# Optimization experiments

Hardware: AMD Instinct MI355X
Metric: run time of the kernel (lower is better)

## Reference

```python
import jax, jax.numpy as jnp
import numpy as np

D = 1024      # n_embd
H = 16        # n_head
HD = D // H   # head_size = 64


def _layernorm(x, g, b, eps=1e-5):
    mu = jnp.mean(x, axis=-1, keepdims=True)
    var = jnp.mean((x - mu) ** 2, axis=-1, keepdims=True)
    return (x - mu) * jax.lax.rsqrt(var + eps) * g + b


def setup_inputs() -> dict:
    key = jax.random.key(0)
    ks = jax.random.split(key, 12)
    s = lambda fan_in: 1.0 / np.sqrt(fan_in)
    inp = {
        "x": jax.random.normal(ks[0], (4, 2048, D), dtype=jnp.float32),
        # attention projections (bias=False in Head), per-head weights fused into [D, D]
        "wq": jax.random.uniform(ks[1], (D, D), jnp.float32, -s(D), s(D)),
        "wk": jax.random.uniform(ks[2], (D, D), jnp.float32, -s(D), s(D)),
        "wv": jax.random.uniform(ks[3], (D, D), jnp.float32, -s(D), s(D)),
        "wo": jax.random.uniform(ks[4], (D, D), jnp.float32, -s(D), s(D)),
        "bo": jax.random.uniform(ks[5], (D,), jnp.float32, -s(D), s(D)),
        # feed-forward: D -> 4D -> D
        "w1": jax.random.uniform(ks[6], (D, 4 * D), jnp.float32, -s(D), s(D)),
        "b1": jax.random.uniform(ks[7], (4 * D,), jnp.float32, -s(D), s(D)),
        "w2": jax.random.uniform(ks[8], (4 * D, D), jnp.float32, -s(4 * D), s(4 * D)),
        "b2": jax.random.uniform(ks[9], (D,), jnp.float32, -s(4 * D), s(4 * D)),
        # layernorms
        "g_ln1": jnp.ones((D,), jnp.float32),
        "b_ln1": jnp.zeros((D,), jnp.float32),
        "g_ln2": jnp.ones((D,), jnp.float32),
        "b_ln2": jnp.zeros((D,), jnp.float32),
    }
    return inp


def reference(x, wq, wk, wv, wo, bo, w1, b1, w2, b2, g_ln1, b_ln1, g_ln2, b_ln2):
    B, T, _ = x.shape
    # --- self-attention on ln1(x) ---
    h = _layernorm(x, g_ln1, b_ln1)
    q = (h @ wq).reshape(B, T, H, HD)
    k = (h @ wk).reshape(B, T, H, HD)
    v = (h @ wv).reshape(B, T, H, HD)
    scores = jnp.einsum("bqhd,bkhd->bhqk", q, k) * (HD ** -0.5)
    causal = jnp.tril(jnp.ones((T, T), dtype=bool))
    scores = jnp.where(causal, scores, -jnp.inf)
    wei = jax.nn.softmax(scores, axis=-1)                    # [B,H,T,T]
    attn = jnp.einsum("bhqk,bkhd->bqhd", wei, v).reshape(B, T, D)
    x = x + attn @ wo + bo
    # --- feed-forward on ln2(x) ---
    h2 = _layernorm(x, g_ln2, b_ln2)
    x = x + jax.nn.relu(h2 @ w1 + b1) @ w2 + b2
    return x
```

## Files before the change

### kernel.cpp

```cpp
#include <hip/hip_runtime.h>
#include <cstdint>

typedef __bf16 bf16x8 __attribute__((ext_vector_type(8)));
typedef float f32x4 __attribute__((ext_vector_type(4)));
typedef unsigned int u32x4 __attribute__((ext_vector_type(4)));
typedef unsigned int u32x2 __attribute__((ext_vector_type(2)));
typedef unsigned short u16x4 __attribute__((ext_vector_type(4)));

#define D_MODEL 1024
#define SEQ     2048
#define NBATCH  4
#define NHEAD   16
#define HDIM    64
#define NTOK    (NBATCH * SEQ)
#define QSCALE  0.18033688011112042f

__device__ __forceinline__ unsigned short f2bf(float f) {
  unsigned int u = __builtin_bit_cast(unsigned int, f);
  u += 0x7FFFu + ((u >> 16) & 1u);
  return (unsigned short)(u >> 16);
}

__device__ __forceinline__ float bf2f(unsigned short s) {
  return __builtin_bit_cast(float, (unsigned int)s << 16);
}

__device__ __forceinline__ bf16x8 load8bf(const unsigned short* p) {
  return __builtin_bit_cast(bf16x8, *(const u32x4*)p);
}

__device__ __forceinline__ f32x4 mfma16(bf16x8 a, bf16x8 b, f32x4 c) {
  return __builtin_amdgcn_mfma_f32_16x16x32_bf16(a, b, c, 0, 0, 0);
}

__device__ __forceinline__ void gload16(const unsigned short* g, unsigned short* l) {
  __builtin_amdgcn_global_load_lds((__attribute__((address_space(1))) void*)g,
                                   (__attribute__((address_space(3))) void*)l, 16, 0, 0);
}

__global__ __launch_bounds__(256) void tcast_all(const float* __restrict__ wq,
                                                 const float* __restrict__ wk,
                                                 const float* __restrict__ wv,
                                                 const float* __restrict__ wo,
                                                 const float* __restrict__ w1,
                                                 const float* __restrict__ w2,
                                                 unsigned short* __restrict__ wqkv_t,
                                                 unsigned short* __restrict__ wo_t,
                                                 unsigned short* __restrict__ w1_t,
                                                 unsigned short* __restrict__ w2_t) {
  const int id = blockIdx.x;
  const float* in; unsigned short* out; int K, N, k0, n0;
  if (id < 4096) {
    const int seg = id >> 10, r = id & 1023;
    in  = seg == 0 ? wq : seg == 1 ? wk : seg == 2 ? wv : wo;
    out = seg == 3 ? wo_t : wqkv_t + (size_t)seg * 1024 * 1024;
    K = 1024; N = 1024; n0 = (r & 31) * 32; k0 = (r >> 5) * 32;
  } else if (id < 8192) {
    const int r = id - 4096;
    in = w1; out = w1_t; K = 1024; N = 4096;
    n0 = (r & 127) * 32; k0 = (r >> 7) * 32;
  } else {
    const int r = id - 8192;
    in = w2; out = w2_t; K = 4096; N = 1024;
    n0 = (r & 31) * 32; k0 = (r >> 5) * 32;
  }
  __shared__ float tile[32][33];
  const int tx = threadIdx.x & 31, ty = threadIdx.x >> 5;
  #pragma unroll
  for (int j = 0; j < 4; ++j)
    tile[ty + 8 * j][tx] = in[(size_t)(k0 + ty + 8 * j) * N + n0 + tx];
  __syncthreads();
  #pragma unroll
  for (int j = 0; j < 4; ++j)
    out[(size_t)(n0 + ty + 8 * j) * K + k0 + tx] = f2bf(tile[tx][ty + 8 * j]);
}

template <int FPIN>
__global__ __launch_bounds__(256) void ln_kernel(const void* __restrict__ xin,
                                                 const float* __restrict__ g,
                                                 const float* __restrict__ bb,
                                                 unsigned short* __restrict__ out) {
  const int row = blockIdx.x, tid = threadIdx.x;
  float4 xv;
  if (FPIN) {
    xv = ((const float4*)((const float*)xin + (size_t)row * D_MODEL))[tid];
  } else {
    const u16x4 bv4 = ((const u16x4*)((const unsigned short*)xin + (size_t)row * D_MODEL))[tid];
    xv.x = bf2f(bv4.x); xv.y = bf2f(bv4.y); xv.z = bf2f(bv4.z); xv.w = bf2f(bv4.w);
  }
  float s  = xv.x + xv.y + xv.z + xv.w;
  float ss = xv.x * xv.x + xv.y * xv.y + xv.z * xv.z + xv.w * xv.w;
  #pragma unroll
  for (int off = 1; off < 64; off <<= 1) { s += __shfl_xor(s, off); ss += __shfl_xor(ss, off); }
  __shared__ float red[8];
  const int wave = tid >> 6, lane = tid & 63;
  if (lane == 0) { red[wave] = s; red[4 + wave] = ss; }
  __syncthreads();
  s  = red[0] + red[1] + red[2] + red[3];
  ss = red[4] + red[5] + red[6] + red[7];
  const float mu   = s * (1.0f / D_MODEL);
  const float var  = ss * (1.0f / D_MODEL) - mu * mu;
  const float rstd = rsqrtf(var + 1e-5f);
  const float4 gv = ((const float4*)g)[tid];
  const float4 bv = ((const float4*)bb)[tid];
  u16x4 o;
  o.x = f2bf((xv.x - mu) * rstd * gv.x + bv.x);
  o.y = f2bf((xv.y - mu) * rstd * gv.y + bv.y);
  o.z = f2bf((xv.z - mu) * rstd * gv.z + bv.z);
  o.w = f2bf((xv.w - mu) * rstd * gv.w + bv.w);
  *(u16x4*)(out + (size_t)row * D_MODEL + tid * 4) = o;
}

template <bool BIAS, bool RELU, int RES, bool OBF>
__global__ __launch_bounds__(256) void gemm_bt(const unsigned short* __restrict__ A,
                                               const unsigned short* __restrict__ Bt,
                                               const float* __restrict__ bias,
                                               const void* __restrict__ res,
                                               void* __restrict__ out,
                                               int M, int N, int K) {
  __shared__ __align__(16) unsigned short As[128 * 64];
  __shared__ __align__(16) unsigned short Bs[128 * 64];
  const int tid  = threadIdx.x;
  const int lin = blockIdx.y * gridDim.x + blockIdx.x;
  const int xcd = lin & 7, idx = lin >> 3;
  const int by = xcd * 8 + (idx & 7);
  const int bx = idx >> 3;
  const int row0 = by * 128, col0 = bx * 128;
  const int wave = tid >> 6, lane = tid & 63;
  const int wm = wave >> 1, wn = wave & 1;
  const int l15 = lane & 15, quad = lane >> 4;
  f32x4 acc[4][4] = {};

  const int tr = tid >> 3;
  const int tc = (tid & 7) ^ (tr & 7);
  const unsigned short* gA = A  + (size_t)(row0 + tr) * K + tc * 8;
  const unsigned short* gB = Bt + (size_t)(col0 + tr) * K + tc * 8;

  const int rowA = (wm * 64 + l15) * 64;
  const int rowB = (wn * 64 + l15) * 64;
  const int swz0 = (quad ^ (l15 & 7)) * 8;
  const int swz1 = ((4 + quad) ^ (l15 & 7)) * 8;

  for (int k0 = 0; k0 < K; k0 += 64) {
    #pragma unroll
    for (int i = 0; i < 4; ++i) {
      gload16(gA + (size_t)(i * 32) * K + k0, As + (i * 256 + tid) * 8);
      gload16(gB + (size_t)(i * 32) * K + k0, Bs + (i * 256 + tid) * 8);
    }
    __syncthreads();
    #pragma unroll
    for (int kf = 0; kf < 2; ++kf) {
      const int swz = kf ? swz1 : swz0;
      bf16x8 af[4], bfr[4];
      #pragma unroll
      for (int t = 0; t < 4; ++t) {
        af[t]  = load8bf(As + rowA + t * 1024 + swz);
        bfr[t] = load8bf(Bs + rowB + t * 1024 + swz);
      }
      #pragma unroll
      for (int i = 0; i < 4; ++i)
        #pragma unroll
        for (int j = 0; j < 4; ++j)
          acc[i][j] = mfma16(af[i], bfr[j], acc[i][j]);
    }
    __syncthreads();
  }

  const size_t rbase = (size_t)row0 + wm * 64 + quad * 4;
  const int cbase = col0 + wn * 64 + l15;
  #pragma unroll
  for (int i = 0; i < 4; ++i) {
    #pragma unroll
    for (int j = 0; j < 4; ++j) {
      const int col = cbase + j * 16;
      const float bval = BIAS ? bias[col] : 0.0f;
      #pragma unroll
      for (int r = 0; r < 4; ++r) {
        const size_t row = rbase + i * 16 + r;
        float v = acc[i][j][r];
        if (BIAS) v += bval;
        if (RELU) v = fmaxf(v, 0.0f);
        if (RES == 1) v += ((const float*)res)[row * N + col];
        if (RES == 2) v += bf2f(((const unsigned short*)res)[row * N + col]);
        if (OBF)  ((unsigned short*)out)[row * N + col] = f2bf(v);
        else      ((float*)out)[row * N + col] = v;
      }
    }
  }
}

__device__ __forceinline__ void stage_half_512(const unsigned short* __restrict__ src,
                                               unsigned short* dst, int ld, int k0,
                                               int h, int tid) {
  #pragma unroll
  for (int l = 0; l < 2; ++l) {
    const int cid = l * 512 + tid;
    const int r = cid >> 3, p = cid & 7, c = p ^ (r & 7);
    gload16(src + (size_t)(h * 128 + r) * ld + k0 + c * 8, dst + h * 8192 + cid * 8);
  }
}

template <bool BIAS, bool RELU, int RES, bool OBF, bool QKV, bool SPLITK>
__global__ __launch_bounds__(512, 2) void gemm256(const unsigned short* __restrict__ A,
                                                  const unsigned short* __restrict__ Bt,
                                                  const float* __restrict__ bias,
                                                  const void* __restrict__ res,
                                                  void* __restrict__ out,
                                                  unsigned short* __restrict__ qb,
                                                  unsigned short* __restrict__ kp,
                                                  unsigned short* __restrict__ vt,
                                                  int M, int N, int K, int lda, int ldb) {
  __shared__ __align__(16) unsigned short lds[2][32768];
  const int tid = threadIdx.x;
  const int lin = blockIdx.y * gridDim.x + blockIdx.x;
  const int xcd = lin & 7, idx = lin >> 3;
  const int by = xcd * 4 + (idx & 3);
  const int bxr = idx >> 2;
  const int ks  = SPLITK ? (bxr >> 2) : 0;
  const int bx  = SPLITK ? (bxr & 3) : bxr;
  const int row0 = by * 256, col0 = bx * 256;
  const int koff = SPLITK ? ks * K : 0;
  const int wave = tid >> 6, lane = tid & 63;
  const int wm = wave >> 2, wn = wave & 3;
  const int l15 = lane & 15, quad = lane >> 4;
  const int swz0 = (quad ^ (l15 & 7)) * 8;
  const int swz1 = ((4 + quad) ^ (l15 & 7)) * 8;

  const unsigned short* gA = A  + (size_t)row0 * lda + koff;
  const unsigned short* gB = Bt + (size_t)col0 * ldb + koff;

  unsigned short* As0 = &lds[0][0];
  unsigned short* Bs0 = &lds[0][16384];
  unsigned short* As1 = &lds[1][0];
  unsigned short* Bs1 = &lds[1][16384];

  f32x4 acc[8][4] = {};
  const int KT = K >> 6;

  stage_half_512(gA, As0, lda, 0, 0, tid);
  stage_half_512(gA, As0, lda, 0, 1, tid);
  stage_half_512(gB, Bs0, ldb, 0, 0, tid);
  stage_half_512(gB, Bs0, ldb, 0, 1, tid);
  if (KT > 1) {
    stage_half_512(gB, Bs1, ldb, 64, 0, tid);
    stage_half_512(gB, Bs1, ldb, 64, 1, tid);
    asm volatile("s_waitcnt vmcnt(4)" ::: "memory");
  } else {
    asm volatile("s_waitcnt vmcnt(0)" ::: "memory");
  }
  asm volatile("s_barrier" ::: "memory");

  for (int t = 0; t < KT; ++t) {
    unsigned short* As  = (t & 1) ? As1 : As0;
    unsigned short* Bs  = (t & 1) ? Bs1 : Bs0;
    unsigned short* Asn = (t & 1) ? As0 : As1;
    const int k1 = (t + 1) << 6, k2 = (t + 2) << 6;
    bf16x8 a0[2][4], b01[2][2], b23[2][2];

    #pragma unroll
    for (int i = 0; i < 4; ++i) {
      const unsigned short* ap = As + (wm * 128 + i * 16 + l15) * 64;
      a0[0][i] = load8bf(ap + swz0);
      a0[1][i] = load8bf(ap + swz1);
    }
    #pragma unroll
    for (int j = 0; j < 2; ++j) {
      const unsigned short* bp = Bs + (wn * 64 + j * 16 + l15) * 64;
      b01[0][j] = load8bf(bp + swz0);
      b01[1][j] = load8bf(bp + swz1);
      const unsigned short* bp2 = Bs + (wn * 64 + 32 + j * 16 + l15) * 64;
      b23[0][j] = load8bf(bp2 + swz0);
      b23[1][j] = load8bf(bp2 + swz1);
    }
    if (t + 1 < KT) {
      stage_half_512(gA, Asn, lda, k1, 0, tid);
      stage_half_512(gA, Asn, lda, k1, 1, tid);
    }
    __builtin_amdgcn_s_setprio(1);
    #pragma unroll
    for (int kf = 0; kf < 2; ++kf)
      #pragma unroll
      for (int i = 0; i < 4; ++i)
        #pragma unroll
        for (int j = 0; j < 2; ++j)
          acc[i][j] = mfma16(a0[kf][i], b01[kf][j], acc[i][j]);
    #pragma unroll
    for (int kf = 0; kf < 2; ++kf)
      #pragma unroll
      for (int i = 0; i < 4; ++i)
        #pragma unroll
        for (int j = 0; j < 2; ++j)
          acc[i][2 + j] = mfma16(a0[kf][i], b23[kf][j], acc[i][2 + j]);
    __builtin_amdgcn_s_setprio(0);
    __builtin_amdgcn_sched_barrier(0);
    asm volatile("s_barrier" ::: "memory");

    #pragma unroll
    for (int i = 0; i < 4; ++i) {
      const unsigned short* ap = As + (wm * 128 + 64 + i * 16 + l15) * 64;
      a0[0][i] = load8bf(ap + swz0);
      a0[1][i] = load8bf(ap + swz1);
    }
    if (t + 2 < KT) {
      stage_half_512(gB, Bs, ldb, k2, 0, tid);
      stage_half_512(gB, Bs, ldb, k2, 1, tid);
    }
    __builtin_amdgcn_s_setprio(1);
    #pragma unroll
    for (int kf = 0; kf < 2; ++kf)
      #pragma unroll
      for (int i = 0; i < 4; ++i)
        #pragma unroll
        for (int j = 0; j < 2; ++j)
          acc[4 + i][2 + j] = mfma16(a0[kf][i], b23[kf][j], acc[4 + i][2 + j]);
    #pragma unroll
    for (int kf = 0; kf < 2; ++kf)
      #pragma unroll
      for (int i = 0; i < 4; ++i)
        #pragma unroll
        for (int j = 0; j < 2; ++j)
          acc[4 + i][j] = mfma16(a0[kf][i], b01[kf][j], acc[4 + i][j]);
    __builtin_amdgcn_s_setprio(0);
    __builtin_amdgcn_sched_barrier(0);
    if (t + 2 < KT) asm volatile("s_waitcnt vmcnt(4)" ::: "memory");
    else            asm volatile("s_waitcnt vmcnt(0)" ::: "memory");
    asm volatile("s_barrier" ::: "memory");
  }

  const size_t rbase = (size_t)row0 + wm * 128 + quad * 4;
  const int cbase = col0 + wn * 64 + l15;
  if (QKV) {
    const int sec = col0 >> 10;
    #pragma unroll
    for (int i = 0; i < 8; ++i) {
      #pragma unroll
      for (int j = 0; j < 4; ++j) {
        const int col = cbase + j * 16;
        if (sec == 0) {
          #pragma unroll
          for (int r = 0; r < 4; ++r) {
            const size_t row = rbase + i * 16 + r;
            qb[row * 1024 + col] = f2bf(acc[i][j][r] * QSCALE);
          }
        } else if (sec == 1) {
          const int c2 = col - 1024, hh = c2 >> 6, d = c2 & 63;
          #pragma unroll
          for (int r = 0; r < 4; ++r) {
            const size_t row = rbase + i * 16 + r;
            const int bb = (int)(row >> 11), tt = (int)(row & 2047);
            kp[(((size_t)(bb * 16 + hh)) * SEQ + tt) * 64 + d] = f2bf(acc[i][j][r]);
          }
        } else {
          const int c2 = col - 2048, hh = c2 >> 6, d = c2 & 63;
          const size_t t0 = rbase + i * 16;
          const int bb = (int)(t0 >> 11);
          u16x4 pk;
          #pragma unroll
          for (int r = 0; r < 4; ++r) pk[r] = f2bf(acc[i][j][r]);
          *(u16x4*)(vt + ((size_t)(bb * 16 + hh) * 64 + d) * SEQ + (t0 & 2047)) = pk;
        }
      }
    }
  } else if (SPLITK) {
    float* po = (float*)out + (size_t)ks * M * N;
    #pragma unroll
    for (int i = 0; i < 8; ++i) {
      #pragma unroll
      for (int j = 0; j < 4; ++j) {
        const int col = cbase + j * 16;
        #pragma unroll
        for (int r = 0; r < 4; ++r) {
          const size_t row = rbase + i * 16 + r;
          po[row * N + col] = acc[i][j][r];
        }
      }
    }
  } else {
    #pragma unroll
    for (int i = 0; i < 8; ++i) {
      #pragma unroll
      for (int j = 0; j < 4; ++j) {
        const int col = cbase + j * 16;
        const float bval = BIAS ? bias[col] : 0.0f;
        #pragma unroll
        for (int r = 0; r < 4; ++r) {
          const size_t row = rbase + i * 16 + r;
          float v = acc[i][j][r];
          if (BIAS) v += bval;
          if (RELU) v = fmaxf(v, 0.0f);
          if (RES == 1) v += ((const float*)res)[row * N + col];
          if (RES == 2) v += bf2f(((const unsigned short*)res)[row * N + col]);
          if (OBF)  ((unsigned short*)out)[row * N + col] = f2bf(v);
          else      ((float*)out)[row * N + col] = v;
        }
      }
    }
  }
  (void)M;
}

__global__ __launch_bounds__(256) void ffn2_reduce(const float* __restrict__ p0,
                                                   const float* __restrict__ p1,
                                                   const float* __restrict__ b2,
                                                   const unsigned short* __restrict__ x1b,
                                                   float* __restrict__ out) {
  const size_t i4 = (size_t)blockIdx.x * 256 + threadIdx.x;
  const float4 a = ((const float4*)p0)[i4];
  const float4 b = ((const float4*)p1)[i4];
  const float4 bi = ((const float4*)b2)[i4 & 255];
  const u16x4 rv = ((const u16x4*)x1b)[i4];
  float4 o;
  o.x = a.x + b.x + bi.x + bf2f(rv.x);
  o.y = a.y + b.y + bi.y + bf2f(rv.y);
  o.z = a.z + b.z + bi.z + bf2f(rv.z);
  o.w = a.w + b.w + bi.w + bf2f(rv.w);
  ((float4*)out)[i4] = o;
}

__global__ __launch_bounds__(256) void attn5(const unsigned short* __restrict__ qb,
                                             const unsigned short* __restrict__ kp,
                                             const unsigned short* __restrict__ vt,
                                             unsigned short* __restrict__ attnb) {
  const int lin = (blockIdx.z * 16 + blockIdx.y) * 8 + blockIdx.x;
  const int xcd = lin & 7, idx = lin >> 3;
  const int bh = xcd * 8 + (idx >> 3);
  const int xb = idx & 7;
  const int b = bh >> 4, h = bh & 15;
  const int tid = threadIdx.x, wave = tid >> 6, lane = tid & 63;
  const int l15 = lane & 15, quad = lane >> 4;
  const size_t tokbase = (size_t)b * SEQ;

  __shared__ __align__(16) unsigned short ks[64 * 64];
  __shared__ __align__(16) unsigned short vts[64 * 64];
  __shared__ __align__(16) unsigned short plds[4][32 * 64];

  const unsigned short* kbase = kp + (size_t)bh * SEQ * HDIM;
  const unsigned short* vbase = vt + (size_t)bh * HDIM * SEQ;

  for (int half = 0; half < 2; ++half) {
    const int qblk = (half == 0) ? (15 - xb) : xb;
    const int qw0 = qblk * 128 + wave * 32;

    bf16x8 qf[2][2];
    #pragma unroll
    for (int qfi = 0; qfi < 2; ++qfi)
      #pragma unroll
      for (int kf = 0; kf < 2; ++kf)
        qf[qfi][kf] = load8bf(qb + (tokbase + qw0 + qfi * 16 + l15) * 1024
                              + h * HDIM + kf * 32 + quad * 8);

    f32x4 o[2][4] = {};
    float lsum[2] = {0.0f, 0.0f};

    const int ntiles = qblk * 2 + 2;
    for (int kt = 0; kt < ntiles; ++kt) {
      const int k0 = kt * 64;
      __syncthreads();
      #pragma unroll
      for (int i = 0; i < 2; ++i) {
        const int cid = i * 256 + tid;
        const int r = cid >> 3, p = cid & 7, c = p ^ (r & 7);
        gload16(kbase + (size_t)(k0 + r) * HDIM + c * 8, ks + cid * 8);
      }
      #pragma unroll
      for (int i = 0; i < 2; ++i) {
        const int cid = i * 256 + tid;
        const int d = cid >> 3, p = cid & 7, c = p ^ (d & 7);
        gload16(vbase + (size_t)d * SEQ + k0 + c * 8, vts + cid * 8);
      }
      __syncthreads();
      if (k0 <= qw0 + 31) {
        f32x4 s[4][2] = {};
        #pragma unroll
        for (int kf = 0; kf < 2; ++kf)
          #pragma unroll
          for (int keyf = 0; keyf < 4; ++keyf) {
            const int row = keyf * 16 + l15;
            const int p = (kf * 4 + quad) ^ (row & 7);
            const bf16x8 kfr = load8bf(ks + row * 64 + p * 8);
            s[keyf][0] = mfma16(kfr, qf[0][kf], s[keyf][0]);
            s[keyf][1] = mfma16(kfr, qf[1][kf], s[keyf][1]);
          }
        #pragma unroll
        for (int qfi = 0; qfi < 2; ++qfi) {
          const int q = qw0 + qfi * 16 + l15;
          const int qloc = qfi * 16 + l15;
          #pragma unroll
          for (int keyf = 0; keyf < 4; ++keyf) {
            unsigned int pw[4];
            #pragma unroll
            for (int r = 0; r < 4; ++r) {
              const int key = k0 + keyf * 16 + quad * 4 + r;
              float p = __builtin_amdgcn_exp2f(s[keyf][qfi][r]);
              p = (key > q) ? 0.0f : p;
              pw[r] = __builtin_bit_cast(unsigned int, p);
              lsum[qfi] += __builtin_bit_cast(float, pw[r] & 0xFFFF0000u);
            }
            u32x2 packed;
            packed.x = (pw[0] >> 16) | (pw[1] & 0xFFFF0000u);
            packed.y = (pw[2] >> 16) | (pw[3] & 0xFFFF0000u);
            const int slot = (keyf * 4 + quad) ^ ((l15 & 7) << 1);
            *(u32x2*)(&plds[wave][qloc * 64 + slot * 4]) = packed;
          }
        }
        __builtin_amdgcn_s_waitcnt(0);
        #pragma unroll
        for (int kf = 0; kf < 2; ++kf) {
          bf16x8 pa[2];
          #pragma unroll
          for (int mf = 0; mf < 2; ++mf) {
            const int lq = mf * 16 + l15;
            const int c = (kf * 4 + quad) ^ (l15 & 7);
            pa[mf] = load8bf(&plds[wave][lq * 64 + c * 8]);
          }
          #pragma unroll
          for (int df = 0; df < 4; ++df) {
            const int row = df * 16 + l15;
            const int p = (kf * 4 + quad) ^ (row & 7);
            const bf16x8 vb = load8bf(vts + row * 64 + p * 8);
            o[0][df] = mfma16(pa[0], vb, o[0][df]);
            o[1][df] = mfma16(pa[1], vb, o[1][df]);
          }
        }
      }
    }
    #pragma unroll
    for (int mf = 0; mf < 2; ++mf) {
      float l = lsum[mf];
      l += __shfl_xor(l, 16);
      l += __shfl_xor(l, 32);
      const float rl = 1.0f / l;
      #pragma unroll
      for (int r = 0; r < 4; ++r) {
        const float rv = __shfl(rl, quad * 4 + r);
        const size_t row = tokbase + qw0 + mf * 16 + quad * 4 + r;
        #pragma unroll
        for (int df = 0; df < 4; ++df)
          attnb[row * D_MODEL + h * HDIM + df * 16 + l15] = f2bf(o[mf][df][r] * rv);
      }
    }
  }
}

extern "C" void kernel_launch(void* const* d_in, const int* in_sizes, int n_in,
                              void* d_out, int out_size, void* d_ws, size_t ws_size,
                              hipStream_t stream) {
  const float* x    = (const float*)d_in[0];
  const float* wq   = (const float*)d_in[1];
  const float* wk   = (const float*)d_in[2];
  const float* wv   = (const float*)d_in[3];
  const float* wo   = (const float*)d_in[4];
  const float* bo   = (const float*)d_in[5];
  const float* w1   = (const float*)d_in[6];
  const float* b1   = (const float*)d_in[7];
  const float* w2   = (const float*)d_in[8];
  const float* b2   = (const float*)d_in[9];
  const float* g1   = (const float*)d_in[10];
  const float* bl1  = (const float*)d_in[11];
  const float* g2   = (const float*)d_in[12];
  const float* bl2  = (const float*)d_in[13];
  float* out = (float*)d_out;

  char* ws = (char*)d_ws;
  size_t off = 0;
  auto alloc = [&](size_t bytes) { char* p = ws + off; off += (bytes + 255) & ~(size_t)255; return p; };
  unsigned short* wqkv_t = (unsigned short*)alloc((size_t)3072 * 1024 * 2);
  unsigned short* wo_t   = (unsigned short*)alloc((size_t)1024 * 1024 * 2);
  unsigned short* w1_t   = (unsigned short*)alloc((size_t)4096 * 1024 * 2);
  unsigned short* w2_t   = (unsigned short*)alloc((size_t)1024 * 4096 * 2);
  unsigned short* h1     = (unsigned short*)alloc((size_t)NTOK * 1024 * 2);
  unsigned short* kpb    = (unsigned short*)alloc((size_t)NTOK * 1024 * 2);
  unsigned short* vtb    = (unsigned short*)alloc((size_t)NTOK * 1024 * 2);
  unsigned short* attnb  = (unsigned short*)alloc((size_t)NTOK * 1024 * 2);
  unsigned short* h2     = (unsigned short*)alloc((size_t)NTOK * 1024 * 2);
  unsigned short* ffn1   = (unsigned short*)alloc((size_t)NTOK * 4096 * 2);
  unsigned short* qb  = attnb;
  unsigned short* x1b = h1;
  float* part = (float*)kpb;

  tcast_all<<<12288, 256, 0, stream>>>(wq, wk, wv, wo, w1, w2,
                                       wqkv_t, wo_t, w1_t, w2_t);
  ln_kernel<1><<<NTOK, 256, 0, stream>>>(x, g1, bl1, h1);
  gemm256<false, false, 0, true, true, false><<<dim3(12, 32), 512, 0, stream>>>(
      h1, wqkv_t, nullptr, nullptr, nullptr, qb, kpb, vtb, NTOK, 3072, 1024, 1024, 1024);
  attn5<<<dim3(SEQ / 256, NHEAD, NBATCH), 256, 0, stream>>>(qb, kpb, vtb, attnb);
  gemm_bt<true, false, 1, true><<<dim3(8, 64), 256, 0, stream>>>(
      attnb, wo_t, bo, x, x1b, NTOK, 1024, 1024);
  ln_kernel<0><<<NTOK, 256, 0, stream>>>(x1b, g2, bl2, h2);
  gemm256<true, true, 0, true, false, false><<<dim3(16, 32), 512, 0, stream>>>(
      h2, w1_t, b1, nullptr, ffn1, nullptr, nullptr, nullptr, NTOK, 4096, 1024, 1024, 1024);
  gemm256<false, false, 0, false, false, true><<<dim3(8, 32), 512, 0, stream>>>(
      ffn1, w2_t, nullptr, nullptr, part, nullptr, nullptr, nullptr,
      NTOK, 1024, 2048, 4096, 4096);
  ffn2_reduce<<<NTOK * 1024 / 4 / 256, 256, 0, stream>>>(
      part, part + (size_t)NTOK * 1024, b2, x1b, out);
  (void)in_sizes; (void)n_in; (void)out_size; (void)ws_size;
}
```

Baseline: 451.6 us.

## Halve GEMM K-tile to 32 with new LDS swizzle to raise occupancy

Result: slower. 1.796 ms (+297.8%).

```diff
diff --git a/kernel.cpp b/kernel.cpp
--- a/kernel.cpp
+++ b/kernel.cpp
@@ -189,19 +189,26 @@
   }
 }
 
-__device__ __forceinline__ void stage_half_512(const unsigned short* __restrict__ src,
-                                               unsigned short* dst, int ld, int k0,
-                                               int h, int tid) {
-  #pragma unroll
-  for (int l = 0; l < 2; ++l) {
-    const int cid = l * 512 + tid;
-    const int r = cid >> 3, p = cid & 7, c = p ^ (r & 7);
-    gload16(src + (size_t)(h * 128 + r) * ld + k0 + c * 8, dst + h * 8192 + cid * 8);
-  }
+__device__ __forceinline__ void stage32(const unsigned short* __restrict__ src,
+                                        unsigned short* dst, int ld, int k0,
+                                        int h, int tid) {
+  const int L = tid >> 3;
+  const int p = tid & 7;
+  const int c = p ^ (L & 7);
+  const int row = h * 128 + L * 2 + (c >> 2);
+  gload16(src + (size_t)row * ld + k0 + (c & 3) * 8, dst + h * 4096 + tid * 8);
+}
+
+__device__ __forceinline__ bf16x8 frag32(const unsigned short* tile, int r0,
+                                         int l15, int quad) {
+  const int row = r0 + l15;
+  const int L = row >> 1;
+  const int p = ((row & 1) * 4 + quad) ^ (L & 7);
+  return load8bf(tile + L * 64 + p * 8);
 }
 
 template <bool BIAS, bool RELU, int RES, bool OBF, bool QKV, bool SPLITK>
-__global__ __launch_bounds__(512, 2) void gemm256(const unsigned short* __restrict__ A,
+__global__ __launch_bounds__(512, 4) void gemm256(const unsigned short* __restrict__ A,
                                                   const unsigned short* __restrict__ Bt,
                                                   const float* __restrict__ bias,
                                                   const void* __restrict__ res,
@@ -210,7 +217,7 @@
                                                   unsigned short* __restrict__ kp,
                                                   unsigned short* __restrict__ vt,
                                                   int M, int N, int K, int lda, int ldb) {
-  __shared__ __align__(16) unsigned short lds[2][32768];
+  __shared__ __align__(16) unsigned short lds[2][16384];
   const int tid = threadIdx.x;
   const int lin = blockIdx.y * gridDim.x + blockIdx.x;
   const int xcd = lin & 7, idx = lin >> 3;
@@ -223,28 +230,26 @@
   const int wave = tid >> 6, lane = tid & 63;
   const int wm = wave >> 2, wn = wave & 3;
   const int l15 = lane & 15, quad = lane >> 4;
-  const int swz0 = (quad ^ (l15 & 7)) * 8;
-  const int swz1 = ((4 + quad) ^ (l15 & 7)) * 8;
 
   const unsigned short* gA = A  + (size_t)row0 * lda + koff;
   const unsigned short* gB = Bt + (size_t)col0 * ldb + koff;
 
   unsigned short* As0 = &lds[0][0];
-  unsigned short* Bs0 = &lds[0][16384];
+  unsigned short* Bs0 = &lds[0][8192];
   unsigned short* As1 = &lds[1][0];
-  unsigned short* Bs1 = &lds[1][16384];
+  unsigned short* Bs1 = &lds[1][8192];
 
   f32x4 acc[8][4] = {};
-  const int KT = K >> 6;
-
-  stage_half_512(gA, As0, lda, 0, 0, tid);
-  stage_half_512(gA, As0, lda, 0, 1, tid);
-  stage_half_512(gB, Bs0, ldb, 0, 0, tid);
-  stage_half_512(gB, Bs0, ldb, 0, 1, tid);
+  const int KT = K >> 5;
+
+  stage32(gA, As0, lda, 0, 0, tid);
+  stage32(gA, As0, lda, 0, 1, tid);
+  stage32(gB, Bs0, ldb, 0, 0, tid);
+  stage32(gB, Bs0, ldb, 0, 1, tid);
   if (KT > 1) {
-    stage_half_512(gB, Bs1, ldb, 64, 0, tid);
-    stage_half_512(gB, Bs1, ldb, 64, 1, tid);
-    asm volatile("s_waitcnt vmcnt(4)" ::: "memory");
+    stage32(gB, Bs1, ldb, 32, 0, tid);
+    stage32(gB, Bs1, ldb, 32, 1, tid);
+    asm volatile("s_waitcnt vmcnt(2)" ::: "memory");
   } else {
     asm volatile("s_waitcnt vmcnt(0)" ::: "memory");
   }
@@ -254,75 +259,42 @@
     unsigned short* As  = (t & 1) ? As1 : As0;
     unsigned short* Bs  = (t & 1) ? Bs1 : Bs0;
     unsigned short* Asn = (t & 1) ? As0 : As1;
-    const int k1 = (t + 1) << 6, k2 = (t + 2) << 6;
-    bf16x8 a0[2][4], b01[2][2], b23[2][2];
-
-    #pragma unroll
-    for (int i = 0; i < 4; ++i) {
-      const unsigned short* ap = As + (wm * 128 + i * 16 + l15) * 64;
-      a0[0][i] = load8bf(ap + swz0);
-      a0[1][i] = load8bf(ap + swz1);
-    }
-    #pragma unroll
-    for (int j = 0; j < 2; ++j) {
-      const unsigned short* bp = Bs + (wn * 64 + j * 16 + l15) * 64;
-      b01[0][j] = load8bf(bp + swz0);
-      b01[1][j] = load8bf(bp + swz1);
-      const unsigned short* bp2 = Bs + (wn * 64 + 32 + j * 16 + l15) * 64;
-      b23[0][j] = load8bf(bp2 + swz0);
-      b23[1][j] = load8bf(bp2 + swz1);
-    }
+    const int k1 = (t + 1) << 5, k2 = (t + 2) << 5;
+    bf16x8 a[4], b[4];
+
+    #pragma unroll
+    for (int i = 0; i < 4; ++i) a[i] = frag32(As, wm * 128 + i * 16, l15, quad);
+    #pragma unroll
+    for (int j = 0; j < 4; ++j) b[j] = frag32(Bs, wn * 64 + j * 16, l15, quad);
     if (t + 1 < KT) {
-      stage_half_512(gA, Asn, lda, k1, 0, tid);
-      stage_half_512(gA, Asn, lda, k1, 1, tid);
+      stage32(gA, Asn, lda, k1, 0, tid);
+      stage32(gA, Asn, lda, k1, 1, tid);
     }
     __builtin_amdgcn_s_setprio(1);
     #pragma unroll
-    for (int kf = 0; kf < 2; ++kf)
-      #pragma unroll
-      for (int i = 0; i < 4; ++i)
-        #pragma unroll
-        for (int j = 0; j < 2; ++j)
-          acc[i][j] = mfma16(a0[kf][i], b01[kf][j], acc[i][j]);
-    #pragma unroll
-    for (int kf = 0; kf < 2; ++kf)
-      #pragma unroll
-      for (int i = 0; i < 4; ++i)
-        #pragma unroll
-        for (int j = 0; j < 2; ++j)
-          acc[i][2 + j] = mfma16(a0[kf][i], b23[kf][j], acc[i][2 + j]);
+    for (int i = 0; i < 4; ++i)
+      #pragma unroll
+      for (int j = 0; j < 4; ++j)
+        acc[i][j] = mfma16(a[i], b[j], acc[i][j]);
     __builtin_amdgcn_s_setprio(0);
     __builtin_amdgcn_sched_barrier(0);
     asm volatile("s_barrier" ::: "memory");
 
     #pragma unroll
-    for (int i = 0; i < 4; ++i) {
-      const unsigned short* ap = As + (wm * 128 + 64 + i * 16 + l15) * 64;
-      a0[0][i] = load8bf(ap + swz0);
-      a0[1][i] = load8bf(ap + swz1);
-    }
+    for (int i = 0; i < 4; ++i) a[i] = frag32(As, wm * 128 + 64 + i * 16, l15, quad);
     if (t + 2 < KT) {
-      stage_half_512(gB, Bs, ldb, k2, 0, tid);
-      stage_half_512(gB, Bs, ldb, k2, 1, tid);
+      stage32(gB, Bs, ldb, k2, 0, tid);
+      stage32(gB, Bs, ldb, k2, 1, tid);
     }
     __builtin_amdgcn_s_setprio(1);
     #pragma unroll
-    for (int kf = 0; kf < 2; ++kf)
-      #pragma unroll
-      for (int i = 0; i < 4; ++i)
-        #pragma unroll
-        for (int j = 0; j < 2; ++j)
-          acc[4 + i][2 + j] = mfma16(a0[kf][i], b23[kf][j], acc[4 + i][2 + j]);
-    #pragma unroll
-    for (int kf = 0; kf < 2; ++kf)
-      #pragma unroll
-      for (int i = 0; i < 4; ++i)
-        #pragma unroll
-        for (int j = 0; j < 2; ++j)
-          acc[4 + i][j] = mfma16(a0[kf][i], b01[kf][j], acc[4 + i][j]);
+    for (int i = 0; i < 4; ++i)
+      #pragma unroll
+      for (int j = 0; j < 4; ++j)
+        acc[4 + i][j] = mfma16(a[i], b[j], acc[4 + i][j]);
     __builtin_amdgcn_s_setprio(0);
     __builtin_amdgcn_sched_barrier(0);
-    if (t + 2 < KT) asm volatile("s_waitcnt vmcnt(4)" ::: "memory");
+    if (t + 2 < KT) asm volatile("s_waitcnt vmcnt(2)" ::: "memory");
     else            asm volatile("s_waitcnt vmcnt(0)" ::: "memory");
     asm volatile("s_barrier" ::: "memory");
   }
```
